# Optimization experiments

Measured on AMD Instinct MI355X. Metric: run time of the kernel, lower is better.

Reference implementation:

```python
import jax, jax.numpy as jnp
import numpy as np

ATT_HEAD = 12
IN_DIM = 768
OUT_DIM = IN_DIM // ATT_HEAD
LEAKY_ALPHA = 0.2
B, N = 8, 512


def setup_inputs() -> dict:
    key = jax.random.key(0)
    ks = jax.random.split(key, 8)
    feat_in = jax.random.normal(ks[0], (B, N, IN_DIM), dtype=jnp.float32)
    adj = jax.random.randint(ks[1], (B, N, N), 0, 2) > 0
    # xavier_uniform for W: fan_in=in_dim, fan_out=out_dim
    lim_W = float(np.sqrt(6.0 / (IN_DIM + OUT_DIM)))
    W = jax.random.uniform(ks[2], (ATT_HEAD, IN_DIM, OUT_DIM), minval=-lim_W, maxval=lim_W, dtype=jnp.float32)
    b = jnp.zeros((OUT_DIM,), dtype=jnp.float32)
    lim_w = float(np.sqrt(6.0 / (OUT_DIM + 1)))
    w_src = jax.random.uniform(ks[3], (ATT_HEAD, OUT_DIM, 1), minval=-lim_w, maxval=lim_w, dtype=jnp.float32)
    w_dst = jax.random.uniform(ks[4], (ATT_HEAD, OUT_DIM, 1), minval=-lim_w, maxval=lim_w, dtype=jnp.float32)
    # xavier_normal for H.weight [in_dim, in_dim]
    std_H = float(np.sqrt(2.0 / (IN_DIM + IN_DIM)))
    H_w = jax.random.normal(ks[5], (IN_DIM, IN_DIM), dtype=jnp.float32) * std_H
    H_b = jax.random.normal(ks[6], (IN_DIM,), dtype=jnp.float32) * 0.01
    return {"feat_in": feat_in, "adj": adj, "W": W, "b": b,
            "w_src": w_src, "w_dst": w_dst, "H_w": H_w, "H_b": H_b}


def reference(feat_in, adj, W, b, w_src, w_dst, H_w, H_b):
    # h: [B, heads, N, out_dim]
    h = jnp.einsum('bnd,ade->bane', feat_in, W)
    th = jnp.tanh(h)
    attn_src = jnp.einsum('bane,aeo->bano', th, w_src)  # [B,A,N,1]
    attn_dst = jnp.einsum('bane,aeo->bano', th, w_dst)  # [B,A,N,1]
    attn = attn_src + jnp.swapaxes(attn_dst, 2, 3)      # [B,A,N,N]
    attn = jnp.where(attn >= 0, attn, LEAKY_ALPHA * attn)
    mask = ~adj[:, None, :, :]                           # [B,1,N,N]
    attn = jnp.where(mask, jnp.float32(-999.0), attn)
    attn = jax.nn.softmax(attn, axis=-1)
    feat_out = jnp.einsum('banm,bame->bane', attn, h) + b
    feat_out = jnp.swapaxes(feat_out, 1, 2).reshape(feat_in.shape[0], feat_in.shape[1], -1)
    feat_out = jax.nn.elu(feat_out)
    gate = jax.nn.sigmoid(feat_in @ H_w.T + H_b)
    return gate * feat_out + (1.0 - gate) * feat_in
```

## Files before the change

### kernel.cpp

```cpp
#include <hip/hip_runtime.h>
#include <hip/hip_bf16.h>

#define BB 8
#define NN 512
#define AH 12
#define DIN 768
#define EE 64
#define MM (BB*NN)
#define YY (BB*AH)
#define LEAKY 0.2f

typedef unsigned short u16;
typedef unsigned int u32;
typedef __attribute__((ext_vector_type(8))) short short8;
typedef __attribute__((ext_vector_type(4))) float f32x4;
typedef __attribute__((ext_vector_type(4))) u32 u32x4;
typedef __attribute__((ext_vector_type(4))) u16 u16x4;

static __device__ __forceinline__ u16 f2bf(float f) {
    u32 u = __builtin_bit_cast(u32, f);
    u32 r = (u + 0x7FFFu + ((u >> 16) & 1u)) >> 16;
    return (u16)r;
}
static __device__ __forceinline__ u32 pk2(float a, float b) {
    return (u32)f2bf(a) | ((u32)f2bf(b) << 16);
}
static __device__ __forceinline__ u32 cvtpk(float a, float b) {
    u32 r;
    asm("v_cvt_pk_bf16_f32 %0, %1, %2" : "=v"(r) : "v"(a), "v"(b));
    return r;
}
static __device__ __forceinline__ float ftanh(float x) {
    x = fminf(fmaxf(x, -15.f), 15.f);
    return 1.f - 2.f / (__expf(2.f * x) + 1.f);
}
static __device__ __forceinline__ float sigm(float z) {
    z = fminf(fmaxf(z, -80.f), 80.f);
    return 1.f / (1.f + __expf(-z));
}
static __device__ __forceinline__ void gl_lds16(const u16* g, u16* l) {
    __builtin_amdgcn_global_load_lds((const __attribute__((address_space(1))) unsigned int*)g,
                                     (__attribute__((address_space(3))) unsigned int*)l,
                                     16, 0, 0);
}

static __device__ __forceinline__ void mfma_probe(int lane, int* prow, int* pcol) {
    int q = lane >> 4, x = lane & 15;
    short8 af, bf;
#pragma unroll
    for (int j = 0; j < 8; j++) {
        int k = q * 8 + j;
        af[j] = (short)f2bf((k < 16) ? (float)(x * 16 + k) : 0.f);
        bf[j] = (short)f2bf((k == x) ? 1.f : 0.f);
    }
    f32x4 d = {};
    d = __builtin_amdgcn_mfma_f32_16x16x32_bf16(af, bf, d, 0, 0, 0);
#pragma unroll
    for (int r = 0; r < 4; r++) {
        int v = (int)(d[r] + 0.5f);
        prow[r] = v >> 4;
        pcol[r] = v & 15;
    }
}

#define N_FEAT (MM*DIN)
#define N_W    (AH*DIN*EE)
#define PACK_BLOCKS (MM/4)
#define FEATV_BLOCKS (N_FEAT/1024)
#define HWBV_BLOCKS (N_W/1024)
#define WT_BLOCKS (AH*(DIN/64))
#define PREP_BLOCKS (PACK_BLOCKS + FEATV_BLOCKS + HWBV_BLOCKS + WT_BLOCKS)

__global__ __launch_bounds__(256) void prep_kernel(const int* __restrict__ adj,
                                                   const float* __restrict__ feat,
                                                   const float* __restrict__ W,
                                                   const float* __restrict__ Hw,
                                                   u32* __restrict__ maskbuf,
                                                   u16* __restrict__ featb,
                                                   u16* __restrict__ Wt,
                                                   u16* __restrict__ Hwb) {
    int blk = blockIdx.x, t = threadIdx.x;
    if (blk < PACK_BLOCKS) {
        int w = t >> 6, ln = t & 63;
        int row = blk * 4 + w;
        const int* ar = adj + (size_t)row * NN;
#pragma unroll
        for (int it = 0; it < 8; it++) {
            unsigned long long bal = __ballot(ar[it * 64 + ln] != 0);
            if (ln == 0) {
                maskbuf[row * 16 + it * 2]     = (u32)bal;
                maskbuf[row * 16 + it * 2 + 1] = (u32)(bal >> 32);
            }
        }
        return;
    }
    blk -= PACK_BLOCKS;
    if (blk < FEATV_BLOCKS) {
        int i = blk * 1024 + t * 4;
        float4 v = *(const float4*)&feat[i];
        u16x4 o = { f2bf(v.x), f2bf(v.y), f2bf(v.z), f2bf(v.w) };
        *(u16x4*)&featb[i] = o;
        return;
    }
    blk -= FEATV_BLOCKS;
    if (blk < HWBV_BLOCKS) {
        int i = blk * 1024 + t * 4;
        float4 v = *(const float4*)&Hw[i];
        u16x4 o = { f2bf(v.x), f2bf(v.y), f2bf(v.z), f2bf(v.w) };
        *(u16x4*)&Hwb[i] = o;
        return;
    }
    blk -= HWBV_BLOCKS;
    __shared__ float tile[64][65];
    int a = blk / (DIN / 64), d0 = (blk % (DIN / 64)) * 64;
    int rl = t >> 4, c4 = (t & 15) * 4;
#pragma unroll
    for (int i = 0; i < 4; i++) {
        int dl = i * 16 + rl;
        float4 v = *(const float4*)&W[((size_t)a * DIN + d0 + dl) * EE + c4];
        tile[dl][c4 + 0] = v.x;
        tile[dl][c4 + 1] = v.y;
        tile[dl][c4 + 2] = v.z;
        tile[dl][c4 + 3] = v.w;
    }
    __syncthreads();
#pragma unroll
    for (int i = 0; i < 4; i++) {
        int e = i * 16 + rl;
        u16x4 o = { f2bf(tile[c4 + 0][e]), f2bf(tile[c4 + 1][e]),
                    f2bf(tile[c4 + 2][e]), f2bf(tile[c4 + 3][e]) };
        *(u16x4*)&Wt[(size_t)a * EE * DIN + (size_t)e * DIN + d0 + c4] = o;
    }
}

__global__ __launch_bounds__(256) void gemm_fused_kernel(const u16* __restrict__ featb,
                                                         const u16* __restrict__ Wt,
                                                         const u16* __restrict__ Hwb,
                                                         const float* __restrict__ wsrc,
                                                         const float* __restrict__ wdst,
                                                         const float* __restrict__ Hb,
                                                         u16* __restrict__ hT,
                                                         float2* __restrict__ Spair,
                                                         float2* __restrict__ Dpair,
                                                         float* __restrict__ Gbuf) {
    __shared__ alignas(16) char smem[49152];
    u16* As0 = (u16*)smem;
    u16* BW0 = (u16*)(smem + 8192);
    u16* BG0 = (u16*)(smem + 16384);
    u16* As1 = (u16*)(smem + 24576);
    u16* BW1 = (u16*)(smem + 32768);
    u16* BG1 = (u16*)(smem + 40960);
    float (*cs)[68] = (float (*)[68])smem;

    int t = threadIdx.x, w = t >> 6, lane = t & 63, q = lane >> 4, x = lane & 15;
    int m0 = blockIdx.x * 64, a = blockIdx.y;

    int wm = w & 1, wn = w >> 1, xr = x & 7;
    int srow = t >> 3;
    int skoff = ((t & 7) ^ (srow & 7)) * 8;
    const u16* Agp  = featb + (size_t)m0 * DIN + srow * DIN + skoff;
    const u16* BWgp = Wt + (size_t)a * EE * DIN + srow * DIN + skoff;
    const u16* BGgp = Hwb + (size_t)(a * EE) * DIN + srow * DIN + skoff;
    int wo = w * 512;
    f32x4 aW00 = {}, aW01 = {}, aW10 = {}, aW11 = {};
    f32x4 aG00 = {}, aG01 = {}, aG10 = {}, aG11 = {};

#define STAGE(A_, BW_, BG_, K_)                                   \
    do {                                                          \
        gl_lds16(Agp + (K_), (A_) + wo);                          \
        gl_lds16(Agp + 32 * DIN + (K_), (A_) + wo + 2048);        \
        gl_lds16(BWgp + (K_), (BW_) + wo);                        \
        gl_lds16(BWgp + 32 * DIN + (K_), (BW_) + wo + 2048);      \
        gl_lds16(BGgp + (K_), (BG_) + wo);                        \
        gl_lds16(BGgp + 32 * DIN + (K_), (BG_) + wo + 2048);      \
    } while (0)

#define COMPUTE(A_, BW_, BG_)                                                       \
    do {                                                                            \
        const u16* ApA  = (A_)  + (wm * 32 + x) * 64;                               \
        const u16* ApBW = (BW_) + (wn * 32 + x) * 64;                               \
        const u16* ApBG = (BG_) + (wn * 32 + x) * 64;                               \
        _Pragma("unroll")                                                           \
        for (int kk = 0; kk < 2; kk++) {                                            \
            int c8 = ((q + kk * 4) ^ xr) * 8;                                       \
            short8 a0 = *(const short8*)(ApA + c8);                                 \
            short8 a1 = *(const short8*)(ApA + 16 * 64 + c8);                       \
            short8 bW0 = *(const short8*)(ApBW + c8);                               \
            short8 bW1 = *(const short8*)(ApBW + 16 * 64 + c8);                     \
            short8 bG0 = *(const short8*)(ApBG + c8);                               \
            short8 bG1 = *(const short8*)(ApBG + 16 * 64 + c8);                     \
            aW00 = __builtin_amdgcn_mfma_f32_16x16x32_bf16(a0, bW0, aW00, 0, 0, 0); \
            aW01 = __builtin_amdgcn_mfma_f32_16x16x32_bf16(a0, bW1, aW01, 0, 0, 0); \
            aW10 = __builtin_amdgcn_mfma_f32_16x16x32_bf16(a1, bW0, aW10, 0, 0, 0); \
            aW11 = __builtin_amdgcn_mfma_f32_16x16x32_bf16(a1, bW1, aW11, 0, 0, 0); \
            aG00 = __builtin_amdgcn_mfma_f32_16x16x32_bf16(a0, bG0, aG00, 0, 0, 0); \
            aG01 = __builtin_amdgcn_mfma_f32_16x16x32_bf16(a0, bG1, aG01, 0, 0, 0); \
            aG10 = __builtin_amdgcn_mfma_f32_16x16x32_bf16(a1, bG0, aG10, 0, 0, 0); \
            aG11 = __builtin_amdgcn_mfma_f32_16x16x32_bf16(a1, bG1, aG11, 0, 0, 0); \
        }                                                                           \
    } while (0)

    STAGE(As0, BW0, BG0, 0);
    __syncthreads();
#pragma unroll 1
    for (int k0 = 0; k0 < DIN; k0 += 128) {
        STAGE(As1, BW1, BG1, k0 + 64);
        COMPUTE(As0, BW0, BG0);
        __syncthreads();
        if (k0 + 128 < DIN) STAGE(As0, BW0, BG0, k0 + 128);
        COMPUTE(As1, BW1, BG1);
        __syncthreads();
    }
#undef STAGE
#undef COMPUTE

    int prow[4], pcol[4];
    mfma_probe(lane, prow, pcol);

#pragma unroll
    for (int r = 0; r < 4; r++) {
        cs[wm * 32 + prow[r]][wn * 32 + pcol[r]]           = aW00[r];
        cs[wm * 32 + prow[r]][wn * 32 + 16 + pcol[r]]      = aW01[r];
        cs[wm * 32 + 16 + prow[r]][wn * 32 + pcol[r]]      = aW10[r];
        cs[wm * 32 + 16 + prow[r]][wn * 32 + 16 + pcol[r]] = aW11[r];
    }
    __syncthreads();

    int b = m0 >> 9;
    int y = b * AH + a;
    int nbase = m0 & 511;
    {
        int kcb = nbase >> 3;
#pragma unroll
        for (int i = 0; i < 2; i++) {
            int idx = i * 256 + t;
            int kcl = idx >> 6, e = idx & 63;
            int r0 = kcl * 8;
            u32x4 wv = { pk2(cs[r0 + 0][e], cs[r0 + 1][e]),
                         pk2(cs[r0 + 2][e], cs[r0 + 3][e]),
                         pk2(cs[r0 + 4][e], cs[r0 + 5][e]),
                         pk2(cs[r0 + 6][e], cs[r0 + 7][e]) };
            *(u32x4*)&hT[((((size_t)y << 6) + kcb + kcl) << 6 | e) * 8] = wv;
        }
    }
    {
        int r = t >> 2, cg = t & 3;
        float s = 0.f, d = 0.f;
#pragma unroll
        for (int i = 0; i < 16; i++) {
            int e2 = cg * 16 + i;
            float th = ftanh(cs[r][e2]);
            s += th * wsrc[a * EE + e2];
            d += th * wdst[a * EE + e2];
        }
        s += __shfl_xor(s, 1); s += __shfl_xor(s, 2);
        d += __shfl_xor(d, 1); d += __shfl_xor(d, 2);
        if (cg == 0) {
            s = fminf(fmaxf(s, -40.f), 40.f);
            d = fminf(fmaxf(d, -40.f), 40.f);
            Spair[y * NN + nbase + r] = make_float2(__expf(s), __expf(0.2f * s));
            Dpair[y * NN + nbase + r] = make_float2(__expf(d), __expf(0.2f * d));
        }
    }
    __syncthreads();

#pragma unroll
    for (int r = 0; r < 4; r++) {
        cs[wm * 32 + prow[r]][wn * 32 + pcol[r]]           = aG00[r];
        cs[wm * 32 + prow[r]][wn * 32 + 16 + pcol[r]]      = aG01[r];
        cs[wm * 32 + 16 + prow[r]][wn * 32 + pcol[r]]      = aG10[r];
        cs[wm * 32 + 16 + prow[r]][wn * 32 + 16 + pcol[r]] = aG11[r];
    }
    __syncthreads();

    {
        int n0 = a * EE;
        float4 hb = *(const float4*)&Hb[n0 + (t & 15) * 4];
#pragma unroll
        for (int p = 0; p < 4; p++) {
            int ml = p * 16 + (t >> 4), c4 = (t & 15) * 4;
            float4 v4 = *(const float4*)&cs[ml][c4];
            size_t idx = (size_t)(m0 + ml) * DIN + n0 + c4;
            float4 o;
            o.x = sigm(v4.x + hb.x);
            o.y = sigm(v4.y + hb.y);
            o.z = sigm(v4.z + hb.z);
            o.w = sigm(v4.w + hb.w);
            *(float4*)&Gbuf[idx] = o;
        }
    }
}

__global__ __launch_bounds__(256) void attn_kernel(const u16* __restrict__ hT,
                                                   const float2* __restrict__ Spair,
                                                   const float2* __restrict__ Dpair,
                                                   const u32* __restrict__ maskbuf,
                                                   const float* __restrict__ bias,
                                                   const float* __restrict__ Gbuf,
                                                   const float* __restrict__ feat,
                                                   float* __restrict__ out) {
    __shared__ alignas(16) float2 sd2[NN];
    __shared__ u32 smask[64][17];
    __shared__ float silv[64];
    __shared__ alignas(16) float cs[64][68];

    int t = threadIdx.x;
    int y = blockIdx.y, bb = y / AH, a = y % AH;
    int i0 = blockIdx.x * 64;
    int w = t >> 6, lane = t & 63, q = lane >> 4, x = lane & 15;

    sd2[t] = Dpair[y * NN + t];
    sd2[t + 256] = Dpair[y * NN + 256 + t];
#pragma unroll
    for (int p = 0; p < 4; p++) {
        int idx = p * 256 + t, r = idx >> 4, c = idx & 15;
        smask[r][c] = maskbuf[((bb << 9) + i0 + r) * 16 + c];
    }
    __syncthreads();

    int rowl = w * 16 + x;
    float2 se = Spair[y * NN + i0 + rowl];
    float es1 = se.x, es2 = se.y;

    u32 anym = 0;
#pragma unroll
    for (int c = 0; c < 16; c++) anym |= smask[rowl][c];
    int uni = (anym == 0);

    const u16* hTy = hT + ((size_t)y << 12) * 8;
    f32x4 acc[4] = {};
    float lsum = 0.f;

#pragma unroll 2
    for (int k0 = 0; k0 < NN; k0 += 32) {
        u32 mb = smask[rowl][k0 >> 5] >> (q * 8);
        const float4* sdp = (const float4*)&sd2[k0 + q * 8];
        float pv[8];
#pragma unroll
        for (int jj = 0; jj < 4; jj++) {
            float4 d4 = sdp[jj];
            float p0 = fmaxf(es1 * d4.x, es2 * d4.y);
            float p1 = fmaxf(es1 * d4.z, es2 * d4.w);
            p0 = ((mb >> (2 * jj)) & 1) ? p0 : 0.f;
            p1 = ((mb >> (2 * jj + 1)) & 1) ? p1 : 0.f;
            p0 = uni ? 1.0f : p0;
            p1 = uni ? 1.0f : p1;
            lsum += p0 + p1;
            pv[2 * jj] = p0;
            pv[2 * jj + 1] = p1;
        }
        short8 af = __builtin_bit_cast(short8, (u32x4){
            cvtpk(pv[0], pv[1]), cvtpk(pv[2], pv[3]),
            cvtpk(pv[4], pv[5]), cvtpk(pv[6], pv[7])});
        const u16* hp = hTy + ((((k0 >> 3) + q) << 6) + x) * 8;
        short8 b0 = *(const short8*)(hp);
        short8 b1 = *(const short8*)(hp + 16 * 8);
        short8 b2 = *(const short8*)(hp + 32 * 8);
        short8 b3 = *(const short8*)(hp + 48 * 8);
        acc[0] = __builtin_amdgcn_mfma_f32_16x16x32_bf16(af, b0, acc[0], 0, 0, 0);
        acc[1] = __builtin_amdgcn_mfma_f32_16x16x32_bf16(af, b1, acc[1], 0, 0, 0);
        acc[2] = __builtin_amdgcn_mfma_f32_16x16x32_bf16(af, b2, acc[2], 0, 0, 0);
        acc[3] = __builtin_amdgcn_mfma_f32_16x16x32_bf16(af, b3, acc[3], 0, 0, 0);
    }

    lsum += __shfl_xor(lsum, 16);
    lsum += __shfl_xor(lsum, 32);
    if (q == 0) silv[rowl] = 1.f / fmaxf(lsum, 1e-30f);

    int prow[4], pcol[4];
    mfma_probe(lane, prow, pcol);
#pragma unroll
    for (int nt = 0; nt < 4; nt++)
#pragma unroll
        for (int r = 0; r < 4; r++)
            cs[w * 16 + prow[r]][nt * 16 + pcol[r]] = acc[nt][r];
    __syncthreads();

    float4 b4 = *(const float4*)&bias[(t & 15) * 4];
#pragma unroll
    for (int p = 0; p < 4; p++) {
        int nl = p * 16 + (t >> 4), e4 = (t & 15) * 4;
        float il = silv[nl];
        float4 c4 = *(const float4*)&cs[nl][e4];
        size_t base = ((size_t)(bb << 9) + i0 + nl) * DIN + a * EE + e4;
        float4 g4 = *(const float4*)&Gbuf[base];
        float4 f4 = *(const float4*)&feat[base];
        float4 o;
        float v, e;
        v = c4.x * il + b4.x; e = v > 0.f ? v : __expf(v) - 1.f; o.x = g4.x * e + (1.f - g4.x) * f4.x;
        v = c4.y * il + b4.y; e = v > 0.f ? v : __expf(v) - 1.f; o.y = g4.y * e + (1.f - g4.y) * f4.y;
        v = c4.z * il + b4.z; e = v > 0.f ? v : __expf(v) - 1.f; o.z = g4.z * e + (1.f - g4.z) * f4.z;
        v = c4.w * il + b4.w; e = v > 0.f ? v : __expf(v) - 1.f; o.w = g4.w * e + (1.f - g4.w) * f4.w;
        *(float4*)&out[base] = o;
    }
}

extern "C" void kernel_launch(void* const* d_in, const int* in_sizes, int n_in,
                              void* d_out, int out_size, void* d_ws, size_t ws_size,
                              hipStream_t stream) {
    const float* feat  = (const float*)d_in[0];
    const int*   adj   = (const int*)  d_in[1];
    const float* W     = (const float*)d_in[2];
    const float* bvec  = (const float*)d_in[3];
    const float* wsrc  = (const float*)d_in[4];
    const float* wdst  = (const float*)d_in[5];
    const float* Hw    = (const float*)d_in[6];
    const float* Hb    = (const float*)d_in[7];
    float* out = (float*)d_out;

    char* ws = (char*)d_ws;
    u16*    featb   = (u16*)(ws);
    u16*    Wt      = (u16*)(ws + 6291456);
    u16*    Hwb     = (u16*)(ws + 7471104);
    u16*    hT      = (u16*)(ws + 8650752);
    float2* Spair   = (float2*)(ws + 14942208);
    float2* Dpair   = (float2*)(ws + 15335424);
    u32*    maskbuf = (u32*)(ws + 15728640);
    float*  Gbuf    = (float*)(ws + 15990784);

    prep_kernel<<<PREP_BLOCKS, 256, 0, stream>>>(
        adj, feat, W, Hw, maskbuf, featb, Wt, Hwb);
    gemm_fused_kernel<<<dim3(MM / 64, AH), 256, 0, stream>>>(
        featb, Wt, Hwb, wsrc, wdst, Hb, hT, Spair, Dpair, Gbuf);
    attn_kernel<<<dim3(NN / 64, YY), 256, 0, stream>>>(
        hT, Spair, Dpair, maskbuf, bvec, Gbuf, feat, out);
}
```

Before: 118.3 us.

## Store gate buffer as fp16 and double-buffer hT tiles through LDS

The sigmoid gate buffer written by the GEMM kernel and read by the attention kernel becomes fp16 instead of fp32, halving that intermediate's global traffic. The attention kernel also stages each 32-row chunk of hT into a double-buffered LDS area using direct global-to-LDS loads, replacing per-lane global reads in the MFMA loop. This adds a block-wide barrier every iteration and reduces gate precision to fp16.

```diff
diff --git a/kernel.cpp b/kernel.cpp
--- a/kernel.cpp
+++ b/kernel.cpp
@@ -1,5 +1,6 @@
 #include <hip/hip_runtime.h>
 #include <hip/hip_bf16.h>
+#include <hip/hip_fp16.h>
 
 #define BB 8
 #define NN 512
@@ -16,6 +17,7 @@
 typedef __attribute__((ext_vector_type(4))) float f32x4;
 typedef __attribute__((ext_vector_type(4))) u32 u32x4;
 typedef __attribute__((ext_vector_type(4))) u16 u16x4;
+typedef __attribute__((ext_vector_type(4))) _Float16 h16x4;
 
 static __device__ __forceinline__ u16 f2bf(float f) {
     u32 u = __builtin_bit_cast(u32, f);
@@ -142,7 +144,7 @@
                                                          u16* __restrict__ hT,
                                                          float2* __restrict__ Spair,
                                                          float2* __restrict__ Dpair,
-                                                         float* __restrict__ Gbuf) {
+                                                         _Float16* __restrict__ Gbuf) {
     __shared__ alignas(16) char smem[49152];
     u16* As0 = (u16*)smem;
     u16* BW0 = (u16*)(smem + 8192);
@@ -281,12 +283,11 @@
             int ml = p * 16 + (t >> 4), c4 = (t & 15) * 4;
             float4 v4 = *(const float4*)&cs[ml][c4];
             size_t idx = (size_t)(m0 + ml) * DIN + n0 + c4;
-            float4 o;
-            o.x = sigm(v4.x + hb.x);
-            o.y = sigm(v4.y + hb.y);
-            o.z = sigm(v4.z + hb.z);
-            o.w = sigm(v4.w + hb.w);
-            *(float4*)&Gbuf[idx] = o;
+            h16x4 o = { (_Float16)sigm(v4.x + hb.x),
+                        (_Float16)sigm(v4.y + hb.y),
+                        (_Float16)sigm(v4.z + hb.z),
+                        (_Float16)sigm(v4.w + hb.w) };
+            *(h16x4*)&Gbuf[idx] = o;
         }
     }
 }
@@ -296,13 +297,14 @@
                                                    const float2* __restrict__ Dpair,
                                                    const u32* __restrict__ maskbuf,
                                                    const float* __restrict__ bias,
-                                                   const float* __restrict__ Gbuf,
+                                                   const _Float16* __restrict__ Gbuf,
                                                    const float* __restrict__ feat,
                                                    float* __restrict__ out) {
     __shared__ alignas(16) float2 sd2[NN];
     __shared__ u32 smask[64][17];
     __shared__ float silv[64];
     __shared__ alignas(16) float cs[64][68];
+    __shared__ alignas(16) u16 Hs[2][2048];
 
     int t = threadIdx.x;
     int y = blockIdx.y, bb = y / AH, a = y % AH;
@@ -316,6 +318,12 @@
         int idx = p * 256 + t, r = idx >> 4, c = idx & 15;
         smask[r][c] = maskbuf[((bb << 9) + i0 + r) * 16 + c];
     }
+
+    const u16* hTy = hT + ((size_t)y << 12) * 8;
+    const u16* gstage = hTy + t * 8;
+    u16* lstage = &Hs[0][0] + w * 512;
+
+    gl_lds16(gstage, lstage);
     __syncthreads();
 
     int rowl = w * 16 + x;
@@ -327,12 +335,15 @@
     for (int c = 0; c < 16; c++) anym |= smask[rowl][c];
     int uni = (anym == 0);
 
-    const u16* hTy = hT + ((size_t)y << 12) * 8;
     f32x4 acc[4] = {};
     float lsum = 0.f;
 
 #pragma unroll 2
     for (int k0 = 0; k0 < NN; k0 += 32) {
+        int cur = (k0 >> 5) & 1;
+        if (k0 + 32 < NN)
+            gl_lds16(gstage + ((k0 + 32) >> 3) * 512, &Hs[cur ^ 1][0] + w * 512);
+
         u32 mb = smask[rowl][k0 >> 5] >> (q * 8);
         const float4* sdp = (const float4*)&sd2[k0 + q * 8];
         float pv[8];
@@ -352,15 +363,16 @@
         short8 af = __builtin_bit_cast(short8, (u32x4){
             cvtpk(pv[0], pv[1]), cvtpk(pv[2], pv[3]),
             cvtpk(pv[4], pv[5]), cvtpk(pv[6], pv[7])});
-        const u16* hp = hTy + ((((k0 >> 3) + q) << 6) + x) * 8;
+        const u16* hp = &Hs[cur][0] + (q * 64 + x) * 8;
         short8 b0 = *(const short8*)(hp);
-        short8 b1 = *(const short8*)(hp + 16 * 8);
-        short8 b2 = *(const short8*)(hp + 32 * 8);
-        short8 b3 = *(const short8*)(hp + 48 * 8);
+        short8 b1 = *(const short8*)(hp + 128);
+        short8 b2 = *(const short8*)(hp + 256);
+        short8 b3 = *(const short8*)(hp + 384);
         acc[0] = __builtin_amdgcn_mfma_f32_16x16x32_bf16(af, b0, acc[0], 0, 0, 0);
         acc[1] = __builtin_amdgcn_mfma_f32_16x16x32_bf16(af, b1, acc[1], 0, 0, 0);
         acc[2] = __builtin_amdgcn_mfma_f32_16x16x32_bf16(af, b2, acc[2], 0, 0, 0);
         acc[3] = __builtin_amdgcn_mfma_f32_16x16x32_bf16(af, b3, acc[3], 0, 0, 0);
+        __syncthreads();
     }
 
     lsum += __shfl_xor(lsum, 16);
@@ -383,14 +395,14 @@
         float il = silv[nl];
         float4 c4 = *(const float4*)&cs[nl][e4];
         size_t base = ((size_t)(bb << 9) + i0 + nl) * DIN + a * EE + e4;
-        float4 g4 = *(const float4*)&Gbuf[base];
+        h16x4 g4 = *(const h16x4*)&Gbuf[base];
         float4 f4 = *(const float4*)&feat[base];
         float4 o;
-        float v, e;
-        v = c4.x * il + b4.x; e = v > 0.f ? v : __expf(v) - 1.f; o.x = g4.x * e + (1.f - g4.x) * f4.x;
-        v = c4.y * il + b4.y; e = v > 0.f ? v : __expf(v) - 1.f; o.y = g4.y * e + (1.f - g4.y) * f4.y;
-        v = c4.z * il + b4.z; e = v > 0.f ? v : __expf(v) - 1.f; o.z = g4.z * e + (1.f - g4.z) * f4.z;
-        v = c4.w * il + b4.w; e = v > 0.f ? v : __expf(v) - 1.f; o.w = g4.w * e + (1.f - g4.w) * f4.w;
+        float v, e, g;
+        v = c4.x * il + b4.x; e = v > 0.f ? v : __expf(v) - 1.f; g = (float)g4.x; o.x = g * e + (1.f - g) * f4.x;
+        v = c4.y * il + b4.y; e = v > 0.f ? v : __expf(v) - 1.f; g = (float)g4.y; o.y = g * e + (1.f - g) * f4.y;
+        v = c4.z * il + b4.z; e = v > 0.f ? v : __expf(v) - 1.f; g = (float)g4.z; o.z = g * e + (1.f - g) * f4.z;
+        v = c4.w * il + b4.w; e = v > 0.f ? v : __expf(v) - 1.f; g = (float)g4.w; o.w = g * e + (1.f - g) * f4.w;
         *(float4*)&out[base] = o;
     }
 }
@@ -416,7 +428,7 @@
     float2* Spair   = (float2*)(ws + 14942208);
     float2* Dpair   = (float2*)(ws + 15335424);
     u32*    maskbuf = (u32*)(ws + 15728640);
-    float*  Gbuf    = (float*)(ws + 15990784);
+    _Float16* Gbuf  = (_Float16*)(ws + 15990784);
 
     prep_kernel<<<PREP_BLOCKS, 256, 0, stream>>>(
         adj, feat, W, Hw, maskbuf, featb, Wt, Hwb);
```

Result: no change. 118.7 us (+0.3%).
